# Kernel optimization log

Hardware: AMD Instinct MI355X
Metric: run time of the kernel (lower is better)

The kernel has to match this reference:

```python
import jax, jax.numpy as jnp
import numpy as np

EPS = 1e-5
DOWNSAMPLE = 0.5


def setup_inputs() -> dict:
    key = jax.random.key(0)
    k1, k2, k3 = jax.random.split(key, 3)
    B, C, H, W = 32, 256, 128, 128
    x = jax.random.normal(k1, (B, C, H, W), dtype=jnp.float32)
    # 1x1 conv: weight [3, C], bias [3]
    conv_w = jax.random.normal(k2, (3, C), dtype=jnp.float32) / np.sqrt(C).astype(np.float32)
    conv_b = jax.random.normal(k3, (3,), dtype=jnp.float32) * 0.01
    return {"x": x, "conv_w": conv_w, "conv_b": conv_b}


def reference(x, conv_w, conv_b):
    B, C, H, W = x.shape
    dh = int(round(H * DOWNSAMPLE))
    dw = int(round(W * DOWNSAMPLE))

    # 1x1 conv producing 3 channels: 2 offset + 1 attention logit
    oa = jnp.einsum('bchw,oc->bohw', x, conv_w) + conv_b[None, :, None, None]
    offset = oa[:, :2]                      # [B,2,H,W]
    attention = jnp.exp(oa[:, 2:3])         # [B,1,H,W]

    # normalized destination coordinates = base grid + offset, clamped
    gy = jnp.broadcast_to((jnp.arange(H, dtype=x.dtype) / H)[:, None], (H, W))
    gx = jnp.broadcast_to((jnp.arange(W, dtype=x.dtype) / W)[None, :], (H, W))
    base = jnp.stack([gy, gx])              # [2,H,W]
    dest = jnp.clip(base[None] + offset, 0.0, 1.0 - EPS)
    dy = jnp.floor(dest[:, 0] * dh)
    dx = jnp.floor(dest[:, 1] * dw)
    cell = (dy * dw + dx).astype(jnp.int32)  # [B,H,W] spatial cell index

    # full flat destination index over (batch, channel, cell)
    b_off = jnp.arange(B, dtype=jnp.int32)[:, None, None, None] * (C * dh * dw)
    c_off = jnp.arange(C, dtype=jnp.int32)[None, :, None, None] * (dh * dw)
    destination = cell[:, None] + b_off + c_off  # [B,C,H,W]

    # scatter-add attention-weighted features
    xw = (x * attention).reshape(-1)
    feat = jax.ops.segment_sum(xw, destination.reshape(-1), num_segments=B * C * dh * dw)

    # scatter-add attention per (batch, cell) for normalization
    a_idx = cell + jnp.arange(B, dtype=jnp.int32)[:, None, None] * (dh * dw)
    att_sum = jax.ops.segment_sum(attention.reshape(-1), a_idx.reshape(-1), num_segments=B * dh * dw) + EPS

    out = feat.reshape(B, C, dh, dw) / att_sum.reshape(B, 1, dh, dw)
    return (out, offset, destination)
```

## Files before the change

kernel.cpp:

```cpp
#include <hip/hip_runtime.h>
#include <math.h>

#define NB 32
#define NC 256
#define NH 128
#define NW 128
#define NDH 64
#define NDW 64
#define NHW (NH * NW)
#define NCELLS (NDH * NDW)
#define OUT0_N (NB * NC * NCELLS)
#define OUT1_BASE OUT0_N
#define OUT1_N (NB * 2 * NHW)
#define OUT2_BASE (OUT1_BASE + OUT1_N)

#define EPSF 1e-5f

typedef unsigned short u16;
typedef unsigned int   u32;

#define WS_CELLS   ((size_t)0)
#define WS_ATTS    (WS_CELLS + (size_t)NB*NHW*2)
#define WS_ECOMB   (WS_ATTS + (size_t)NB*NHW*4)
#define WS_ASUM    (WS_ECOMB + (size_t)NB*NHW*4)

__device__ inline u16 f32_to_bf16_rn(float f) {
    const u32 u = __float_as_uint(f);
    return (u16)((u + 0x7FFFu + ((u >> 16) & 1u)) >> 16);
}

__global__ __launch_bounds__(256) void k_conv(
    const float* __restrict__ x, const float* __restrict__ cw,
    const float* __restrict__ cb, float* __restrict__ out,
    u16* __restrict__ cells, float* __restrict__ atts)
{
    __shared__ float cwS[3][NC];
    __shared__ float red[256][13];
    __shared__ int   cellv[64];

    const int t    = threadIdx.x;
    const int blk  = blockIdx.x;
    const int b    = blk >> 8;
    const int tile = blk & 255;
    const int h    = tile >> 1;
    const int w0   = (tile & 1) << 6;
    const int pixbase = h * NW + w0;

    cwS[0][t] = cw[t];
    cwS[1][t] = cw[NC + t];
    cwS[2][t] = cw[2 * NC + t];
    __syncthreads();

    const int ct = t >> 4;
    const int pg = (t & 15) << 2;
    const float* xb = x + (size_t)b * NC * NHW + pixbase + pg;

    float p00 = 0, p01 = 0, p02 = 0;
    float p10 = 0, p11 = 0, p12 = 0;
    float p20 = 0, p21 = 0, p22 = 0;
    float p30 = 0, p31 = 0, p32 = 0;

    #pragma unroll
    for (int i = 0; i < 16; ++i) {
        const int c = (i << 4) + ct;
        const float4 xv = *reinterpret_cast<const float4*>(xb + (size_t)c * NHW);
        const float wc0 = cwS[0][c], wc1 = cwS[1][c], wc2 = cwS[2][c];
        p00 += xv.x * wc0; p01 += xv.x * wc1; p02 += xv.x * wc2;
        p10 += xv.y * wc0; p11 += xv.y * wc1; p12 += xv.y * wc2;
        p20 += xv.z * wc0; p21 += xv.z * wc1; p22 += xv.z * wc2;
        p30 += xv.w * wc0; p31 += xv.w * wc1; p32 += xv.w * wc2;
    }

    red[t][0]  = p00; red[t][1]  = p01; red[t][2]  = p02;
    red[t][3]  = p10; red[t][4]  = p11; red[t][5]  = p12;
    red[t][6]  = p20; red[t][7]  = p21; red[t][8]  = p22;
    red[t][9]  = p30; red[t][10] = p31; red[t][11] = p32;
    __syncthreads();

    if (t < 64) {
        const int px   = t;
        const int row0 = px >> 2;
        const int col  = (px & 3) * 3;
        float s0 = 0, s1 = 0, s2 = 0;
        #pragma unroll
        for (int j = 0; j < 16; ++j) {
            const int r = row0 + (j << 4);
            s0 += red[r][col];
            s1 += red[r][col + 1];
            s2 += red[r][col + 2];
        }
        const float off0 = s0 + cb[0];
        const float off1 = s1 + cb[1];
        const float att  = expf(s2 + cb[2]);

        const float gy = (float)h * (1.0f / NH);
        const float gx = (float)(w0 + px) * (1.0f / NW);
        const float dyf = fminf(fmaxf(gy + off0, 0.0f), 0.99999f);
        const float dxf = fminf(fmaxf(gx + off1, 0.0f), 0.99999f);
        const int dy = (int)floorf(dyf * (float)NDH);
        const int dx = (int)floorf(dxf * (float)NDW);
        const int cell = dy * NDW + dx;

        cellv[px] = cell;
        cells[b * NHW + pixbase + px] = (u16)cell;
        atts [b * NHW + pixbase + px] = att;

        const int o1 = OUT1_BASE + b * 2 * NHW + pixbase + px;
        out[o1]       = off0;
        out[o1 + NHW] = off1;
    }
    __syncthreads();

    const int  c0 = cellv[pg], c1 = cellv[pg + 1], c2 = cellv[pg + 2], c3 = cellv[pg + 3];
    float* __restrict__ dst = out + OUT2_BASE;
    #pragma unroll
    for (int i = 0; i < 16; ++i) {
        const int c = (i << 4) + ct;
        const int basec = (b * NC + c) * NCELLS;
        float4 dv;
        dv.x = (float)(basec + c0);
        dv.y = (float)(basec + c1);
        dv.z = (float)(basec + c2);
        dv.w = (float)(basec + c3);
        *reinterpret_cast<float4*>(dst + (size_t)(b * NC + c) * NHW + pixbase + pg) = dv;
    }
}

__global__ __launch_bounds__(1024) void k_sort(
    const u16* __restrict__ cells, const float* __restrict__ atts,
    u32* __restrict__ ecomb, float* __restrict__ asum)
{
    __shared__ u32   hist[NCELLS];
    __shared__ float as_[NCELLS];
    __shared__ u32   ts[1024];

    const int t = threadIdx.x;
    const int b = blockIdx.x;
    const u16*   cb_ = cells + b * NHW;
    const float* ab_ = atts + b * NHW;

    #pragma unroll
    for (int j = 0; j < 4; ++j) { hist[t + 1024 * j] = 0u; as_[t + 1024 * j] = 0.f; }
    __syncthreads();

    #pragma unroll
    for (int j = 0; j < 16; ++j) {
        const int p  = t + 1024 * j;
        const int cl = cb_[p];
        atomicAdd(&hist[cl], 1u);
        atomicAdd(&as_[cl], ab_[p]);
    }
    __syncthreads();

    const u32 h0 = hist[4 * t], h1 = hist[4 * t + 1], h2 = hist[4 * t + 2], h3 = hist[4 * t + 3];
    const u32 T  = h0 + h1 + h2 + h3;
    ts[t] = T;
    __syncthreads();
    for (int off = 1; off < 1024; off <<= 1) {
        const u32 v = (t >= off) ? ts[t - off] : 0u;
        __syncthreads();
        ts[t] += v;
        __syncthreads();
    }
    const u32 base = ts[t] - T;
    hist[4 * t]     = base;
    hist[4 * t + 1] = base + h0;
    hist[4 * t + 2] = base + h0 + h1;
    hist[4 * t + 3] = base + h0 + h1 + h2;

    #pragma unroll
    for (int j = 0; j < 4; ++j)
        asum[b * NCELLS + t + 1024 * j] = as_[t + 1024 * j];
    __syncthreads();

    #pragma unroll
    for (int j = 0; j < 16; ++j) {
        const int p  = t + 1024 * j;
        const int cl = cb_[p];
        const u32 pos = atomicAdd(&hist[cl], 1u);
        ecomb[b * NHW + pos] = ((u32)cl << 16) | (u32)p;
    }
}

__global__ __launch_bounds__(256) void k_gather(
    const float* __restrict__ x, const float* __restrict__ atts,
    const u32* __restrict__ ecomb, const float* __restrict__ asum,
    float* __restrict__ out)
{
    __shared__ u16   xpl[NHW];
    __shared__ float acc[NCELLS];

    const int t   = threadIdx.x;
    const int blk = blockIdx.x;
    const int b   = blk >> 8;
    const int c   = blk & 255;

    const float4* xp4  = reinterpret_cast<const float4*>(x + (size_t)(b * NC + c) * NHW);
    const float4* at4  = reinterpret_cast<const float4*>(atts + b * NHW);
    float4*       acc4 = reinterpret_cast<float4*>(acc);

    #pragma unroll
    for (int k = 0; k < 16; ++k) {
        const int idx = t + 256 * k;
        const float4 xv = xp4[idx];
        const float4 av = at4[idx];
        const u32 lo = (u32)f32_to_bf16_rn(xv.x * av.x)
                     | ((u32)f32_to_bf16_rn(xv.y * av.y) << 16);
        const u32 hi = (u32)f32_to_bf16_rn(xv.z * av.z)
                     | ((u32)f32_to_bf16_rn(xv.w * av.w) << 16);
        *reinterpret_cast<uint2*>(&xpl[idx * 4]) = make_uint2(lo, hi);
    }
    const float4 z4 = make_float4(0.f, 0.f, 0.f, 0.f);
    #pragma unroll
    for (int k = 0; k < 4; ++k) acc4[t + 256 * k] = z4;
    __syncthreads();

    const u32* el = ecomb + b * NHW + t * 64;
    float s   = 0.f;
    int   cur = (int)(el[0] >> 16);

    #define BF16V(E) __uint_as_float((u32)xpl[(E) & 0xFFFFu] << 16)
    #define ACCUM(E, V)                                            \
        {                                                          \
            const int cl_ = (int)((E) >> 16);                      \
            if (cl_ != cur) { atomicAdd(&acc[cur], s); s = 0.f; cur = cl_; } \
            s += (V);                                              \
        }

    for (int ch = 0; ch < 8; ++ch) {
        const uint4 e0 = *reinterpret_cast<const uint4*>(el + ch * 8);
        const uint4 e1 = *reinterpret_cast<const uint4*>(el + ch * 8 + 4);
        const float v0 = BF16V(e0.x);
        const float v1 = BF16V(e0.y);
        const float v2 = BF16V(e0.z);
        const float v3 = BF16V(e0.w);
        const float v4 = BF16V(e1.x);
        const float v5 = BF16V(e1.y);
        const float v6 = BF16V(e1.z);
        const float v7 = BF16V(e1.w);
        ACCUM(e0.x, v0); ACCUM(e0.y, v1); ACCUM(e0.z, v2); ACCUM(e0.w, v3);
        ACCUM(e1.x, v4); ACCUM(e1.y, v5); ACCUM(e1.z, v6); ACCUM(e1.w, v7);
    }
    atomicAdd(&acc[cur], s);
    #undef ACCUM
    #undef BF16V
    __syncthreads();

    const float4* as4 = reinterpret_cast<const float4*>(asum + b * NCELLS);
    float4* ob4 = reinterpret_cast<float4*>(out + (size_t)(b * NC + c) * NCELLS);
    #pragma unroll
    for (int k = 0; k < 4; ++k) {
        float4 a = acc4[t + 256 * k];
        const float4 sv = as4[t + 256 * k];
        a.x /= (sv.x + EPSF);
        a.y /= (sv.y + EPSF);
        a.z /= (sv.z + EPSF);
        a.w /= (sv.w + EPSF);
        ob4[t + 256 * k] = a;
    }
}

extern "C" void kernel_launch(void* const* d_in, const int* in_sizes, int n_in,
                              void* d_out, int out_size, void* d_ws, size_t ws_size,
                              hipStream_t stream)
{
    (void)in_sizes; (void)n_in; (void)out_size; (void)ws_size;
    const float* x  = (const float*)d_in[0];
    const float* cw = (const float*)d_in[1];
    const float* cb = (const float*)d_in[2];
    float* out = (float*)d_out;
    char*  ws  = (char*)d_ws;

    u16*   cells = (u16*)  (ws + WS_CELLS);
    float* atts  = (float*)(ws + WS_ATTS);
    u32*   ecomb = (u32*)  (ws + WS_ECOMB);
    float* asum  = (float*)(ws + WS_ASUM);

    k_conv  <<<dim3(NB * 256), dim3(256),  0, stream>>>(x, cw, cb, out, cells, atts);
    k_sort  <<<dim3(NB),       dim3(1024), 0, stream>>>(cells, atts, ecomb, asum);
    k_gather<<<dim3(NB * NC),  dim3(256),  0, stream>>>(x, atts, ecomb, asum, out);
}
```

Measured before the change: 442.6 us.

## Split destination write into own kernel, wave-aggregate sort atomics, widen gather blocks

The destination-index write moves out of the conv kernel into a separate k_dest kernel, so k_conv only computes cells and attention. In k_sort, runs of equal cells within a wavefront are reduced with shuffle-based segmented scans, so only one shared-memory atomic is issued per run in both the histogram and the scatter pass. k_gather now uses 512 threads per block, each thread walking two 16-element segments of the sorted list to gain more parallelism and overlap. The cost is an extra kernel launch and a second pass over the cell array, plus more shuffle work in the sort.

```diff
diff --git a/kernel.cpp b/kernel.cpp
--- a/kernel.cpp
+++ b/kernel.cpp
@@ -24,19 +24,18 @@
 #define WS_ECOMB   (WS_ATTS + (size_t)NB*NHW*4)
 #define WS_ASUM    (WS_ECOMB + (size_t)NB*NHW*4)
 
-__device__ inline u16 f32_to_bf16_rn(float f) {
+__device__ __forceinline__ u16 f32_to_bf16_rn(float f) {
     const u32 u = __float_as_uint(f);
     return (u16)((u + 0x7FFFu + ((u >> 16) & 1u)) >> 16);
 }
 
-__global__ __launch_bounds__(256) void k_conv(
+__global__ __launch_bounds__(256) void k_cells(
     const float* __restrict__ x, const float* __restrict__ cw,
     const float* __restrict__ cb, float* __restrict__ out,
     u16* __restrict__ cells, float* __restrict__ atts)
 {
     __shared__ float cwS[3][NC];
     __shared__ float red[256][13];
-    __shared__ int   cellv[64];
 
     const int t    = threadIdx.x;
     const int blk  = blockIdx.x;
@@ -101,7 +100,6 @@
         const int dx = (int)floorf(dxf * (float)NDW);
         const int cell = dy * NDW + dx;
 
-        cellv[px] = cell;
         cells[b * NHW + pixbase + px] = (u16)cell;
         atts [b * NHW + pixbase + px] = att;
 
@@ -109,9 +107,123 @@
         out[o1]       = off0;
         out[o1 + NHW] = off1;
     }
-    __syncthreads();
-
-    const int  c0 = cellv[pg], c1 = cellv[pg + 1], c2 = cellv[pg + 2], c3 = cellv[pg + 3];
+}
+
+__global__ __launch_bounds__(1024) void k_sort(
+    const u16* __restrict__ cells, const float* __restrict__ atts,
+    u32* __restrict__ ecomb, float* __restrict__ asum)
+{
+    __shared__ u32   hist[NCELLS];
+    __shared__ float as_[NCELLS];
+    __shared__ u32   ts[1024];
+
+    const int t    = threadIdx.x;
+    const int b    = blockIdx.x;
+    const int lane = t & 63;
+    const u16*   cb_ = cells + b * NHW;
+    const float* ab_ = atts + b * NHW;
+
+    #pragma unroll
+    for (int j = 0; j < 4; ++j) { hist[t + 1024 * j] = 0u; as_[t + 1024 * j] = 0.f; }
+    __syncthreads();
+
+    #pragma unroll
+    for (int j = 0; j < 16; ++j) {
+        const int p  = t + 1024 * j;
+        const int cl = cb_[p];
+        const float av = ab_[p];
+
+        const int clp = __shfl_up(cl, 1);
+        const int cln = __shfl_down(cl, 1);
+        const bool head = (lane == 0)  || (cl != clp);
+        int  tl  = (lane == 63) ? 1 : (cl != cln ? 1 : 0);
+        float s  = av;
+        int   cnt = 1;
+        #pragma unroll
+        for (int d = 1; d < 64; d <<= 1) {
+            const float s2 = __shfl_down(s, d);
+            const int   c2 = __shfl_down(cnt, d);
+            const int   t2 = __shfl_down(tl, d);
+            if (!tl && lane + d < 64) { s += s2; cnt += c2; tl = t2; }
+        }
+        if (head) {
+            atomicAdd(&hist[cl], (u32)cnt);
+            atomicAdd(&as_[cl], s);
+        }
+    }
+    __syncthreads();
+
+    const u32 h0 = hist[4 * t], h1 = hist[4 * t + 1], h2 = hist[4 * t + 2], h3 = hist[4 * t + 3];
+    const u32 T  = h0 + h1 + h2 + h3;
+    ts[t] = T;
+    __syncthreads();
+    for (int off = 1; off < 1024; off <<= 1) {
+        const u32 v = (t >= off) ? ts[t - off] : 0u;
+        __syncthreads();
+        ts[t] += v;
+        __syncthreads();
+    }
+    const u32 base0 = ts[t] - T;
+    hist[4 * t]     = base0;
+    hist[4 * t + 1] = base0 + h0;
+    hist[4 * t + 2] = base0 + h0 + h1;
+    hist[4 * t + 3] = base0 + h0 + h1 + h2;
+
+    #pragma unroll
+    for (int j = 0; j < 4; ++j)
+        asum[b * NCELLS + t + 1024 * j] = as_[t + 1024 * j];
+    __syncthreads();
+
+    #pragma unroll
+    for (int j = 0; j < 16; ++j) {
+        const int p  = t + 1024 * j;
+        const int cl = cb_[p];
+
+        const int clp = __shfl_up(cl, 1);
+        const int cln = __shfl_down(cl, 1);
+        const bool head = (lane == 0)  || (cl != clp);
+        int tl  = (lane == 63) ? 1 : (cl != cln ? 1 : 0);
+        int cnt = 1;
+        #pragma unroll
+        for (int d = 1; d < 64; d <<= 1) {
+            const int c2 = __shfl_down(cnt, d);
+            const int t2 = __shfl_down(tl, d);
+            if (!tl && lane + d < 64) { cnt += c2; tl = t2; }
+        }
+        int hl = head ? lane : 0;
+        #pragma unroll
+        for (int d = 1; d < 64; d <<= 1) {
+            const int h2 = __shfl_up(hl, d);
+            if (lane >= d) hl = max(hl, h2);
+        }
+        int base = 0;
+        if (head) base = (int)atomicAdd(&hist[cl], (u32)cnt);
+        base = __shfl(base, hl);
+        const u32 pos = (u32)(base + (lane - hl));
+        ecomb[b * NHW + pos] = ((u32)cl << 16) | (u32)p;
+    }
+}
+
+__global__ __launch_bounds__(256) void k_dest(
+    const u16* __restrict__ cells, float* __restrict__ out)
+{
+    __shared__ u16 cl_s[64];
+
+    const int t    = threadIdx.x;
+    const int blk  = blockIdx.x;
+    const int b    = blk >> 8;
+    const int tile = blk & 255;
+    const int h    = tile >> 1;
+    const int w0   = (tile & 1) << 6;
+    const int pixbase = h * NW + w0;
+
+    if (t < 64) cl_s[t] = cells[b * NHW + pixbase + t];
+    __syncthreads();
+
+    const int ct = t >> 4;
+    const int pg = (t & 15) << 2;
+    const int c0 = cl_s[pg], c1 = cl_s[pg + 1], c2 = cl_s[pg + 2], c3 = cl_s[pg + 3];
+
     float* __restrict__ dst = out + OUT2_BASE;
     #pragma unroll
     for (int i = 0; i < 16; ++i) {
@@ -126,63 +238,15 @@
     }
 }
 
-__global__ __launch_bounds__(1024) void k_sort(
-    const u16* __restrict__ cells, const float* __restrict__ atts,
-    u32* __restrict__ ecomb, float* __restrict__ asum)
-{
-    __shared__ u32   hist[NCELLS];
-    __shared__ float as_[NCELLS];
-    __shared__ u32   ts[1024];
-
-    const int t = threadIdx.x;
-    const int b = blockIdx.x;
-    const u16*   cb_ = cells + b * NHW;
-    const float* ab_ = atts + b * NHW;
-
-    #pragma unroll
-    for (int j = 0; j < 4; ++j) { hist[t + 1024 * j] = 0u; as_[t + 1024 * j] = 0.f; }
-    __syncthreads();
-
-    #pragma unroll
-    for (int j = 0; j < 16; ++j) {
-        const int p  = t + 1024 * j;
-        const int cl = cb_[p];
-        atomicAdd(&hist[cl], 1u);
-        atomicAdd(&as_[cl], ab_[p]);
-    }
-    __syncthreads();
-
-    const u32 h0 = hist[4 * t], h1 = hist[4 * t + 1], h2 = hist[4 * t + 2], h3 = hist[4 * t + 3];
-    const u32 T  = h0 + h1 + h2 + h3;
-    ts[t] = T;
-    __syncthreads();
-    for (int off = 1; off < 1024; off <<= 1) {
-        const u32 v = (t >= off) ? ts[t - off] : 0u;
-        __syncthreads();
-        ts[t] += v;
-        __syncthreads();
-    }
-    const u32 base = ts[t] - T;
-    hist[4 * t]     = base;
-    hist[4 * t + 1] = base + h0;
-    hist[4 * t + 2] = base + h0 + h1;
-    hist[4 * t + 3] = base + h0 + h1 + h2;
-
-    #pragma unroll
-    for (int j = 0; j < 4; ++j)
-        asum[b * NCELLS + t + 1024 * j] = as_[t + 1024 * j];
-    __syncthreads();
-
-    #pragma unroll
-    for (int j = 0; j < 16; ++j) {
-        const int p  = t + 1024 * j;
-        const int cl = cb_[p];
-        const u32 pos = atomicAdd(&hist[cl], 1u);
-        ecomb[b * NHW + pos] = ((u32)cl << 16) | (u32)p;
-    }
-}
-
-__global__ __launch_bounds__(256) void k_gather(
+#define BF16V(E) __uint_as_float((u32)xpl[(E) & 0xFFFFu] << 16)
+#define ACCUM(CUR, S, E, V)                                                   \
+    {                                                                         \
+        const int cl_ = (int)((E) >> 16);                                     \
+        if (cl_ != (CUR)) { atomicAdd(&acc[(CUR)], (S)); (S) = 0.f; (CUR) = cl_; } \
+        (S) += (V);                                                           \
+    }
+
+__global__ __launch_bounds__(512) void k_gather(
     const float* __restrict__ x, const float* __restrict__ atts,
     const u32* __restrict__ ecomb, const float* __restrict__ asum,
     float* __restrict__ out)
@@ -200,8 +264,8 @@
     float4*       acc4 = reinterpret_cast<float4*>(acc);
 
     #pragma unroll
-    for (int k = 0; k < 16; ++k) {
-        const int idx = t + 256 * k;
+    for (int k = 0; k < 8; ++k) {
+        const int idx = t + 512 * k;
         const float4 xv = xp4[idx];
         const float4 av = at4[idx];
         const u32 lo = (u32)f32_to_bf16_rn(xv.x * av.x)
@@ -212,51 +276,41 @@
     }
     const float4 z4 = make_float4(0.f, 0.f, 0.f, 0.f);
     #pragma unroll
-    for (int k = 0; k < 4; ++k) acc4[t + 256 * k] = z4;
-    __syncthreads();
-
-    const u32* el = ecomb + b * NHW + t * 64;
-    float s   = 0.f;
-    int   cur = (int)(el[0] >> 16);
-
-    #define BF16V(E) __uint_as_float((u32)xpl[(E) & 0xFFFFu] << 16)
-    #define ACCUM(E, V)                                            \
-        {                                                          \
-            const int cl_ = (int)((E) >> 16);                      \
-            if (cl_ != cur) { atomicAdd(&acc[cur], s); s = 0.f; cur = cl_; } \
-            s += (V);                                              \
-        }
-
-    for (int ch = 0; ch < 8; ++ch) {
-        const uint4 e0 = *reinterpret_cast<const uint4*>(el + ch * 8);
-        const uint4 e1 = *reinterpret_cast<const uint4*>(el + ch * 8 + 4);
-        const float v0 = BF16V(e0.x);
-        const float v1 = BF16V(e0.y);
-        const float v2 = BF16V(e0.z);
-        const float v3 = BF16V(e0.w);
-        const float v4 = BF16V(e1.x);
-        const float v5 = BF16V(e1.y);
-        const float v6 = BF16V(e1.z);
-        const float v7 = BF16V(e1.w);
-        ACCUM(e0.x, v0); ACCUM(e0.y, v1); ACCUM(e0.z, v2); ACCUM(e0.w, v3);
-        ACCUM(e1.x, v4); ACCUM(e1.y, v5); ACCUM(e1.z, v6); ACCUM(e1.w, v7);
-    }
-    atomicAdd(&acc[cur], s);
-    #undef ACCUM
-    #undef BF16V
+    for (int k = 0; k < 2; ++k) acc4[t + 512 * k] = z4;
+    __syncthreads();
+
+    const u32* el = ecomb + b * NHW + t * 32;
+    {
+        float s0 = 0.f, s1 = 0.f;
+        int   c0 = (int)(el[0]  >> 16);
+        int   c1 = (int)(el[16] >> 16);
+        #pragma unroll
+        for (int ch = 0; ch < 4; ++ch) {
+            const uint4 e0 = *reinterpret_cast<const uint4*>(el + ch * 4);
+            const uint4 e1 = *reinterpret_cast<const uint4*>(el + 16 + ch * 4);
+            const float v00 = BF16V(e0.x), v01 = BF16V(e0.y), v02 = BF16V(e0.z), v03 = BF16V(e0.w);
+            const float v10 = BF16V(e1.x), v11 = BF16V(e1.y), v12 = BF16V(e1.z), v13 = BF16V(e1.w);
+            ACCUM(c0, s0, e0.x, v00); ACCUM(c1, s1, e1.x, v10);
+            ACCUM(c0, s0, e0.y, v01); ACCUM(c1, s1, e1.y, v11);
+            ACCUM(c0, s0, e0.z, v02); ACCUM(c1, s1, e1.z, v12);
+            ACCUM(c0, s0, e0.w, v03); ACCUM(c1, s1, e1.w, v13);
+        }
+        atomicAdd(&acc[c0], s0);
+        atomicAdd(&acc[c1], s1);
+    }
     __syncthreads();
 
     const float4* as4 = reinterpret_cast<const float4*>(asum + b * NCELLS);
     float4* ob4 = reinterpret_cast<float4*>(out + (size_t)(b * NC + c) * NCELLS);
     #pragma unroll
-    for (int k = 0; k < 4; ++k) {
-        float4 a = acc4[t + 256 * k];
-        const float4 sv = as4[t + 256 * k];
+    for (int k = 0; k < 2; ++k) {
+        float4 a = acc4[t + 512 * k];
+        const float4 sv = as4[t + 512 * k];
         a.x /= (sv.x + EPSF);
         a.y /= (sv.y + EPSF);
         a.z /= (sv.z + EPSF);
         a.w /= (sv.w + EPSF);
-        ob4[t + 256 * k] = a;
+        ob4[t + 512 * k] = a;
     }
 }
 
@@ -276,7 +330,8 @@
     u32*   ecomb = (u32*)  (ws + WS_ECOMB);
     float* asum  = (float*)(ws + WS_ASUM);
 
-    k_conv  <<<dim3(NB * 256), dim3(256),  0, stream>>>(x, cw, cb, out, cells, atts);
+    k_cells <<<dim3(NB * 256), dim3(256),  0, stream>>>(x, cw, cb, out, cells, atts);
     k_sort  <<<dim3(NB),       dim3(1024), 0, stream>>>(cells, atts, ecomb, asum);
-    k_gather<<<dim3(NB * NC),  dim3(256),  0, stream>>>(x, atts, ecomb, asum, out);
-}
+    k_dest  <<<dim3(NB * 256), dim3(256),  0, stream>>>(cells, out);
+    k_gather<<<dim3(NB * NC),  dim3(512),  0, stream>>>(x, atts, ecomb, asum, out);
+}
```

Result: slower. 474.6 us (+7.2%).

## Move destination-index writes into gather kernel and interleave four accumulation streams

Applied to the files above, without the earlier changes.

The large destination-index output write moves out of the conv kernel into the per-(batch,channel) gather kernel, which now reads the cell array and writes it before the scatter phase. The conv kernel becomes lighter and the big store can overlap with the gather's LDS staging. The gather's sorted-run accumulation is also split into four independent chains per thread for more ILP. The cost is extra cell reads per gather block and more atomics at chain boundaries.

```diff
diff --git a/kernel.cpp b/kernel.cpp
--- a/kernel.cpp
+++ b/kernel.cpp
@@ -24,19 +24,18 @@
 #define WS_ECOMB   (WS_ATTS + (size_t)NB*NHW*4)
 #define WS_ASUM    (WS_ECOMB + (size_t)NB*NHW*4)
 
-__device__ inline u16 f32_to_bf16_rn(float f) {
+__device__ __forceinline__ u16 f32_to_bf16_rn(float f) {
     const u32 u = __float_as_uint(f);
     return (u16)((u + 0x7FFFu + ((u >> 16) & 1u)) >> 16);
 }
 
-__global__ __launch_bounds__(256) void k_conv(
+__global__ __launch_bounds__(256) void k_cells(
     const float* __restrict__ x, const float* __restrict__ cw,
     const float* __restrict__ cb, float* __restrict__ out,
     u16* __restrict__ cells, float* __restrict__ atts)
 {
     __shared__ float cwS[3][NC];
     __shared__ float red[256][13];
-    __shared__ int   cellv[64];
 
     const int t    = threadIdx.x;
     const int blk  = blockIdx.x;
@@ -101,28 +100,12 @@
         const int dx = (int)floorf(dxf * (float)NDW);
         const int cell = dy * NDW + dx;
 
-        cellv[px] = cell;
         cells[b * NHW + pixbase + px] = (u16)cell;
         atts [b * NHW + pixbase + px] = att;
 
         const int o1 = OUT1_BASE + b * 2 * NHW + pixbase + px;
         out[o1]       = off0;
         out[o1 + NHW] = off1;
-    }
-    __syncthreads();
-
-    const int  c0 = cellv[pg], c1 = cellv[pg + 1], c2 = cellv[pg + 2], c3 = cellv[pg + 3];
-    float* __restrict__ dst = out + OUT2_BASE;
-    #pragma unroll
-    for (int i = 0; i < 16; ++i) {
-        const int c = (i << 4) + ct;
-        const int basec = (b * NC + c) * NCELLS;
-        float4 dv;
-        dv.x = (float)(basec + c0);
-        dv.y = (float)(basec + c1);
-        dv.z = (float)(basec + c2);
-        dv.w = (float)(basec + c3);
-        *reinterpret_cast<float4*>(dst + (size_t)(b * NC + c) * NHW + pixbase + pg) = dv;
     }
 }
 
@@ -182,10 +165,18 @@
     }
 }
 
-__global__ __launch_bounds__(256) void k_gather(
+#define BF16V(E) __uint_as_float((u32)xpl[(E) & 0xFFFFu] << 16)
+#define ACCUM(CUR, S, E, V)                                                   \
+    {                                                                         \
+        const int cl_ = (int)((E) >> 16);                                     \
+        if (cl_ != (CUR)) { atomicAdd(&acc[(CUR)], (S)); (S) = 0.f; (CUR) = cl_; } \
+        (S) += (V);                                                           \
+    }
+
+__global__ __launch_bounds__(256) void k_gdest(
     const float* __restrict__ x, const float* __restrict__ atts,
-    const u32* __restrict__ ecomb, const float* __restrict__ asum,
-    float* __restrict__ out)
+    const u16* __restrict__ cells, const u32* __restrict__ ecomb,
+    const float* __restrict__ asum, float* __restrict__ out)
 {
     __shared__ u16   xpl[NHW];
     __shared__ float acc[NCELLS];
@@ -213,37 +204,53 @@
     const float4 z4 = make_float4(0.f, 0.f, 0.f, 0.f);
     #pragma unroll
     for (int k = 0; k < 4; ++k) acc4[t + 256 * k] = z4;
-    __syncthreads();
-
-    const u32* el = ecomb + b * NHW + t * 64;
-    float s   = 0.f;
-    int   cur = (int)(el[0] >> 16);
-
-    #define BF16V(E) __uint_as_float((u32)xpl[(E) & 0xFFFFu] << 16)
-    #define ACCUM(E, V)                                            \
-        {                                                          \
-            const int cl_ = (int)((E) >> 16);                      \
-            if (cl_ != cur) { atomicAdd(&acc[cur], s); s = 0.f; cur = cl_; } \
-            s += (V);                                              \
+
+    {
+        const uint2* cl2 = reinterpret_cast<const uint2*>(cells + b * NHW);
+        float4* dst4 = reinterpret_cast<float4*>(out + OUT2_BASE + (size_t)(b * NC + c) * NHW);
+        const int basec = (b * NC + c) * NCELLS;
+        #pragma unroll
+        for (int k = 0; k < 16; ++k) {
+            const int idx = t + 256 * k;
+            const uint2 cc = cl2[idx];
+            float4 dv;
+            dv.x = (float)(basec + (int)(cc.x & 0xFFFFu));
+            dv.y = (float)(basec + (int)(cc.x >> 16));
+            dv.z = (float)(basec + (int)(cc.y & 0xFFFFu));
+            dv.w = (float)(basec + (int)(cc.y >> 16));
+            dst4[idx] = dv;
         }
-
-    for (int ch = 0; ch < 8; ++ch) {
-        const uint4 e0 = *reinterpret_cast<const uint4*>(el + ch * 8);
-        const uint4 e1 = *reinterpret_cast<const uint4*>(el + ch * 8 + 4);
-        const float v0 = BF16V(e0.x);
-        const float v1 = BF16V(e0.y);
-        const float v2 = BF16V(e0.z);
-        const float v3 = BF16V(e0.w);
-        const float v4 = BF16V(e1.x);
-        const float v5 = BF16V(e1.y);
-        const float v6 = BF16V(e1.z);
-        const float v7 = BF16V(e1.w);
-        ACCUM(e0.x, v0); ACCUM(e0.y, v1); ACCUM(e0.z, v2); ACCUM(e0.w, v3);
-        ACCUM(e1.x, v4); ACCUM(e1.y, v5); ACCUM(e1.z, v6); ACCUM(e1.w, v7);
-    }
-    atomicAdd(&acc[cur], s);
-    #undef ACCUM
-    #undef BF16V
+    }
+    __syncthreads();
+
+    {
+        const u32* el = ecomb + b * NHW + t * 64;
+        float s0 = 0.f, s1 = 0.f, s2 = 0.f, s3 = 0.f;
+        int   c0 = (int)(el[0]  >> 16);
+        int   c1 = (int)(el[16] >> 16);
+        int   c2 = (int)(el[32] >> 16);
+        int   c3 = (int)(el[48] >> 16);
+
+        #pragma unroll
+        for (int ch = 0; ch < 4; ++ch) {
+            const uint4 e0 = *reinterpret_cast<const uint4*>(el + ch * 4);
+            const uint4 e1 = *reinterpret_cast<const uint4*>(el + 16 + ch * 4);
+            const uint4 e2 = *reinterpret_cast<const uint4*>(el + 32 + ch * 4);
+            const uint4 e3 = *reinterpret_cast<const uint4*>(el + 48 + ch * 4);
+            const float v00 = BF16V(e0.x), v01 = BF16V(e0.y), v02 = BF16V(e0.z), v03 = BF16V(e0.w);
+            const float v10 = BF16V(e1.x), v11 = BF16V(e1.y), v12 = BF16V(e1.z), v13 = BF16V(e1.w);
+            const float v20 = BF16V(e2.x), v21 = BF16V(e2.y), v22 = BF16V(e2.z), v23 = BF16V(e2.w);
+            const float v30 = BF16V(e3.x), v31 = BF16V(e3.y), v32 = BF16V(e3.z), v33 = BF16V(e3.w);
+            ACCUM(c0, s0, e0.x, v00); ACCUM(c1, s1, e1.x, v10); ACCUM(c2, s2, e2.x, v20); ACCUM(c3, s3, e3.x, v30);
+            ACCUM(c0, s0, e0.y, v01); ACCUM(c1, s1, e1.y, v11); ACCUM(c2, s2, e2.y, v21); ACCUM(c3, s3, e3.y, v31);
+            ACCUM(c0, s0, e0.z, v02); ACCUM(c1, s1, e1.z, v12); ACCUM(c2, s2, e2.z, v22); ACCUM(c3, s3, e3.z, v32);
+            ACCUM(c0, s0, e0.w, v03); ACCUM(c1, s1, e1.w, v13); ACCUM(c2, s2, e2.w, v23); ACCUM(c3, s3, e3.w, v33);
+        }
+        atomicAdd(&acc[c0], s0);
+        atomicAdd(&acc[c1], s1);
+        atomicAdd(&acc[c2], s2);
+        atomicAdd(&acc[c3], s3);
+    }
     __syncthreads();
 
     const float4* as4 = reinterpret_cast<const float4*>(asum + b * NCELLS);
@@ -276,7 +283,7 @@
     u32*   ecomb = (u32*)  (ws + WS_ECOMB);
     float* asum  = (float*)(ws + WS_ASUM);
 
-    k_conv  <<<dim3(NB * 256), dim3(256),  0, stream>>>(x, cw, cb, out, cells, atts);
-    k_sort  <<<dim3(NB),       dim3(1024), 0, stream>>>(cells, atts, ecomb, asum);
-    k_gather<<<dim3(NB * NC),  dim3(256),  0, stream>>>(x, atts, ecomb, asum, out);
-}
+    k_cells<<<dim3(NB * 256), dim3(256),  0, stream>>>(x, cw, cb, out, cells, atts);
+    k_sort <<<dim3(NB),       dim3(1024), 0, stream>>>(cells, atts, ecomb, asum);
+    k_gdest<<<dim3(NB * NC),  dim3(256),  0, stream>>>(x, atts, cells, ecomb, asum, out);
+}
```

New measurement: 476.7 us. 1.08x slower.
